# Kernel optimization log

Measured on AMD Instinct MI355X. Metric: run time of the kernel, lower is better.

## Reference

```python
import jax, jax.numpy as jnp
import numpy as np

B, N, K, ACT = 8192, 784, 16, 4  # batch, qubits/pixels, Kraus rank, d^2
L = N - 1


def setup_inputs() -> dict:
    key = jax.random.key(0)
    kx, kr, ki = jax.random.split(key, 3)
    X = jax.random.normal(kx, (B, N, 2), dtype=jnp.float32)
    # Random TPCP maps per layer via QR of a (K*4, 4) complex Gaussian (isometry method)
    M = (jax.random.normal(kr, (L, K * ACT, ACT), dtype=jnp.float32)
         + 1j * jax.random.normal(ki, (L, K * ACT, ACT), dtype=jnp.float32))
    Q, _ = jnp.linalg.qr(M)  # (L, K*4, 4), Q^dag Q = I per layer
    Kops = Q.reshape(L, K, ACT, ACT)
    return {
        "X": X,
        "kraus_real": jnp.real(Kops).astype(jnp.float32),
        "kraus_imag": jnp.imag(Kops).astype(jnp.float32),
    }


def _get_rho(x):
    # x: (B, 2) real -> pure-state density matrix (B, 2, 2)
    return jnp.einsum('bi,bj->bij', x, x)


def _tensor_product(r1, r2):
    # (B,2,2) x (B,2,2) -> (B,4,4)
    b = r1.shape[0]
    return jnp.einsum('bij,bkl->bikjl', r1, r2).reshape(b, ACT, ACT)


def _forward_layer(rho, Kl):
    # sum_k K_k rho K_k^dag ; Kl: (K,4,4), rho: (B,4,4)
    return jnp.einsum('kab,nbc,kdc->nad', Kl, rho, jnp.conj(Kl))


def _partial0(rho):
    # trace out qubit 0: (B,4,4) -> (B,2,2)
    b = rho.shape[0]
    return jnp.einsum('nacad->ncd', rho.reshape(b, 2, 2, 2, 2))


def reference(X, kraus_real, kraus_imag):
    kraus = kraus_real + 1j * kraus_imag          # (L, K, 4, 4) complex64
    X = X / jnp.linalg.norm(X, axis=-1, keepdims=True)
    Xc = X.astype(kraus.dtype)
    rho = _tensor_product(_get_rho(Xc[:, 0]), _get_rho(Xc[:, 1]))  # (B,4,4)

    def step(rho, xs):
        Kl, x = xs                                # (K,4,4), (B,2)
        rho = _forward_layer(rho, Kl)
        rho = _tensor_product(_partial0(rho), _get_rho(x))
        return rho, None

    xs = (kraus[:-1], jnp.swapaxes(Xc[:, 2:], 0, 1))  # (L-1,K,4,4), (L-1,B,2)
    rho, _ = jax.lax.scan(step, rho, xs)
    rho = _forward_layer(rho, kraus[-1])
    res = _partial0(rho)[:, 0, 0]                 # (B,) diagonal element, real-valued
    return jnp.real(res)
```

## Files before the change

kernel.cpp:

```cpp
#include <hip/hip_runtime.h>

#define L_LAYERS 783
#define L_PAD    784
#define B_BATCH  8192
#define N_SITES  784
#define K_KRAUS  16

#define SEGF     14
#define GF       56
#define TCW      36
#define PW       12

__global__ void __launch_bounds__(256)
build_T(const float* __restrict__ kr, const float* __restrict__ ki,
        float* __restrict__ Tc) {
    __shared__ float lr[K_KRAUS * 16];
    __shared__ float li[K_KRAUS * 16];
    __shared__ float gr[32], gi[32];
    int l = blockIdx.x;
    int t = threadIdx.x;
    float* o = Tc + (size_t)l * TCW;

    if (l >= L_LAYERS) {
        if (t < 12) {
            int r3 = t >> 2, col = t & 3;
            int row = (r3 == 0) ? 0 : r3 + 1;
            o[t]      = (col == row) ? 1.f : 0.f;
            o[12 + t] = 0.f;
            o[24 + t] = 0.f;
        }
        return;
    }

    lr[t] = kr[(size_t)l * 256 + t];
    li[t] = ki[(size_t)l * 256 + t];
    __syncthreads();

    if (t < 128) {
        int e = t >> 2, chunk = t & 3;
        int ci = e >> 4;
        int c = 0, d = ci;
        int m = (e >> 2) & 3, q = e & 3;
        int i1 = m >> 1, j1 = m & 1, i2 = q >> 1, j2 = q & 1;
        int off1 = c * 4 + 2 * i1 + i2;
        int off2 = d * 4 + 2 * j1 + j2;
        float ar = 0.f, ai = 0.f;
        #pragma unroll
        for (int kk = 0; kk < 4; ++kk) {
            int kbase = (chunk * 4 + kk) * 16;
            #pragma unroll
            for (int a = 0; a < 2; ++a) {
                int x1 = kbase + a * 8 + off1;
                int x2 = kbase + a * 8 + off2;
                float k1r = lr[x1], k1i = li[x1];
                float k2r = lr[x2], k2i = li[x2];
                ar += k1r * k2r + k1i * k2i;
                ai += k1i * k2r - k1r * k2i;
            }
        }
        ar += __shfl_xor(ar, 1); ar += __shfl_xor(ar, 2);
        ai += __shfl_xor(ai, 1); ai += __shfl_xor(ai, 2);
        if (chunk == 0) { gr[e] = ar; gi[e] = ai; }
    }
    __syncthreads();

    if (t < 12) {
        int r3 = t >> 2, col = t & 3;
        int row = (r3 == 0) ? 0 : r3 + 1;
        int ci = (row == 0) ? 0 : 1;
        int base = ci * 16;
        float Ur[4], Ui[4];
        #pragma unroll
        for (int q = 0; q < 4; ++q) {
            if (col == 0)      { Ur[q] = gr[base + q];      Ui[q] = gi[base + q]; }
            else if (col == 1) { Ur[q] = gr[base + 12 + q]; Ui[q] = gi[base + 12 + q]; }
            else {
                float t1r = gr[base + 4 + q], t1i = gi[base + 4 + q];
                float t2r = gr[base + 8 + q], t2i = gi[base + 8 + q];
                if (col == 2) { Ur[q] = t1r + t2r;    Ui[q] = t1i + t2i; }
                else          { Ur[q] = -(t1i - t2i); Ui[q] = t1r - t2r; }
            }
        }
        float A, Bc, Cc;
        if (row == 3) { A = Ui[0]; Bc = Ui[1] + Ui[2]; Cc = Ui[3]; }
        else          { A = Ur[0]; Bc = Ur[1] + Ur[2]; Cc = Ur[3]; }
        o[t]      = Cc;
        o[12 + t] = A - Cc;
        o[24 + t] = Bc;
    }
}

__global__ void __launch_bounds__(256, 4)
seg_fused(const float* __restrict__ X, const float* __restrict__ Tc,
          float* __restrict__ P) {
    __shared__ float2 xxs[256 * SEGF];
    int t  = threadIdx.x;
    int s  = blockIdx.y;
    int ls = s * SEGF;
    int b0 = blockIdx.x * 256;
    const float* tl0 = Tc + (size_t)ls * TCW;
    const float2* Xp = (const float2*)X;

    #pragma unroll
    for (int e = 0; e < SEGF; ++e) {
        int idx  = t + e * 256;
        int row  = idx / SEGF;
        int col  = idx - row * SEGF;
        int site = ls + 1 + col;
        site = site < (N_SITES - 1) ? site : (N_SITES - 1);
        float2 xv = Xp[(size_t)(b0 + row) * N_SITES + site];
        float inv = __builtin_amdgcn_rcpf(fmaf(xv.x, xv.x, xv.y * xv.y));
        xxs[row * SEGF + col] = make_float2(xv.x * xv.x * inv, xv.x * xv.y * inv);
    }
    __syncthreads();

    float pA[12], pB[12];
    #pragma unroll
    for (int i = 0; i < 12; ++i) pA[i] = 0.f;
    pA[0] = 1.f; pA[6] = 1.f; pA[11] = 1.f;

#define STEP(SRC, DST, I)                                                       \
    {                                                                           \
        const float* tl = tl0 + (I) * TCW;               \
        float2 xx = xxs[t * SEGF + (I)];                                        \
        float R[12];                                                            \
        _Pragma("unroll")                                                       \
        for (int e = 0; e < 12; ++e)                                            \
            R[e] = fmaf(tl[24 + e], xx.y, fmaf(tl[12 + e], xx.x, tl[e]));       \
        _Pragma("unroll")                                                       \
        for (int r = 0; r < 3; ++r) {                                           \
            float Rd = R[r * 4 + 0] - R[r * 4 + 1];                             \
            float R1 = R[r * 4 + 1];                                            \
            _Pragma("unroll")                                                   \
            for (int cc = 0; cc < 4; ++cc) {                                    \
                float base = (cc < 2) ? R1 : 0.f;                               \
                DST[r * 4 + cc] =                                               \
                    fmaf(Rd, SRC[cc],                                           \
                    fmaf(R[r * 4 + 2], SRC[4 + cc],                             \
                    fmaf(R[r * 4 + 3], SRC[8 + cc], base)));                    \
            }                                                                   \
        }                                                                       \
    }

    #pragma unroll
    for (int i = 0; i < SEGF; i += 2) {
        STEP(pA, pB, i);
        STEP(pB, pA, i + 1);
    }
#undef STEP

    int b = b0 + t;
    #pragma unroll
    for (int i = 0; i < 12; ++i)
        P[((size_t)(s * PW + i)) * B_BATCH + b] = pA[i];
}

__global__ void __launch_bounds__(256)
combine56(const float* __restrict__ X, const float* __restrict__ P,
          float* __restrict__ out) {
    __shared__ float q[256][13];
    int t = threadIdx.x;
    int j = t >> 5, bl = t & 31;
    int b = blockIdx.x * 32 + bl;

    float qa[12], qb[12];
    #pragma unroll
    for (int i = 0; i < 12; ++i) qa[i] = 0.f;
    qa[0] = 1.f; qa[6] = 1.f; qa[11] = 1.f;

#define CSTEP(SRC, DST, K)                                                      \
    {                                                                           \
        float m[12];                                                            \
        _Pragma("unroll")                                                       \
        for (int i = 0; i < 12; ++i)                                            \
            m[i] = P[((size_t)((j * 7 + (K)) * PW + i)) * B_BATCH + b];         \
        _Pragma("unroll")                                                       \
        for (int r = 0; r < 3; ++r) {                                           \
            float Rd = m[r * 4 + 0] - m[r * 4 + 1];                             \
            float R1 = m[r * 4 + 1];                                            \
            _Pragma("unroll")                                                   \
            for (int cc = 0; cc < 4; ++cc) {                                    \
                float base = (cc < 2) ? R1 : 0.f;                               \
                DST[r * 4 + cc] =                                               \
                    fmaf(Rd, SRC[cc],                                           \
                    fmaf(m[r * 4 + 2], SRC[4 + cc],                             \
                    fmaf(m[r * 4 + 3], SRC[8 + cc], base)));                    \
            }                                                                   \
        }                                                                       \
    }
    CSTEP(qa, qb, 0); CSTEP(qb, qa, 1);
    CSTEP(qa, qb, 2); CSTEP(qb, qa, 3);
    CSTEP(qa, qb, 4); CSTEP(qb, qa, 5);
    CSTEP(qa, qb, 6);
#undef CSTEP

    #pragma unroll
    for (int i = 0; i < 12; ++i) q[t][i] = qb[i];
    __syncthreads();

    if (t < 32) {
        int b2 = blockIdx.x * 32 + t;
        const float2* Xp = (const float2*)X;
        float2 xv = Xp[(size_t)b2 * N_SITES];
        float inv = __builtin_amdgcn_rcpf(fmaf(xv.x, xv.x, xv.y * xv.y));
        float v0 = xv.x * xv.x * inv;
        float v1 = xv.y * xv.y * inv;
        float v2 = xv.x * xv.y * inv;
        float v3 = 0.f;
        #pragma unroll
        for (int jj = 0; jj < 8; ++jj) {
            const float* qq = q[jj * 32 + t];
            float n0 = fmaf(qq[0], v0, fmaf(qq[1], v1, fmaf(qq[2],  v2, qq[3]  * v3)));
            float n2 = fmaf(qq[4], v0, fmaf(qq[5], v1, fmaf(qq[6],  v2, qq[7]  * v3)));
            float n3 = fmaf(qq[8], v0, fmaf(qq[9], v1, fmaf(qq[10], v2, qq[11] * v3)));
            float n1 = (v0 + v1) - n0;
            v0 = n0; v1 = n1; v2 = n2; v3 = n3;
        }
        out[b2] = v0;
    }
}

extern "C" void kernel_launch(void* const* d_in, const int* in_sizes, int n_in,
                              void* d_out, int out_size, void* d_ws, size_t ws_size,
                              hipStream_t stream) {
    const float* X  = (const float*)d_in[0];
    const float* kr = (const float*)d_in[1];
    const float* ki = (const float*)d_in[2];
    float* out = (float*)d_out;

    float* Tc = (float*)d_ws;
    const size_t Tb = ((size_t)L_PAD * TCW * sizeof(float) + 255) & ~(size_t)255;
    float* P = (float*)((char*)d_ws + Tb);

    build_T<<<L_PAD, 256, 0, stream>>>(kr, ki, Tc);

    dim3 gs(B_BATCH / 256, GF);
    seg_fused<<<gs, 256, 0, stream>>>(X, Tc, P);

    combine56<<<B_BATCH / 32, 256, 0, stream>>>(X, P, out);
}
```

Before: 37.93 us.

## Split each segment across two half-blocks and store partial products as float4

Each block now handles 128 batch rows. The two halves of the block each chain 7 layers of the 14-layer segment, so the serial dependency per thread is halved. The second half's partial product goes through shared memory and is multiplied in by the first half. P is stored and read as float4 rows in both seg_fused and combine56, and launch bounds are raised to 7 blocks per SM for occupancy. This adds a second barrier and leaves half the threads idle during the final merge.

```diff
diff --git a/kernel.cpp b/kernel.cpp
--- a/kernel.cpp
+++ b/kernel.cpp
@@ -7,9 +7,10 @@
 #define K_KRAUS  16
 
 #define SEGF     14
+#define HSEG     7
 #define GF       56
 #define TCW      36
-#define PW       12
+#define BPB      128
 
 __global__ void __launch_bounds__(256)
 build_T(const float* __restrict__ kr, const float* __restrict__ ki,
@@ -90,29 +91,33 @@
     }
 }
 
-__global__ void __launch_bounds__(256, 4)
+__global__ void __launch_bounds__(256, 7)
 seg_fused(const float* __restrict__ X, const float* __restrict__ Tc,
           float* __restrict__ P) {
-    __shared__ float2 xxs[256 * SEGF];
+    __shared__ float2 xxs[BPB * 15];
+    __shared__ float  qx[BPB][13];
     int t  = threadIdx.x;
     int s  = blockIdx.y;
     int ls = s * SEGF;
-    int b0 = blockIdx.x * 256;
-    const float* tl0 = Tc + (size_t)ls * TCW;
+    int b0 = blockIdx.x * BPB;
     const float2* Xp = (const float2*)X;
 
     #pragma unroll
-    for (int e = 0; e < SEGF; ++e) {
+    for (int e = 0; e < 7; ++e) {
         int idx  = t + e * 256;
-        int row  = idx / SEGF;
-        int col  = idx - row * SEGF;
+        int row  = idx / 14;
+        int col  = idx - row * 14;
         int site = ls + 1 + col;
         site = site < (N_SITES - 1) ? site : (N_SITES - 1);
         float2 xv = Xp[(size_t)(b0 + row) * N_SITES + site];
         float inv = __builtin_amdgcn_rcpf(fmaf(xv.x, xv.x, xv.y * xv.y));
-        xxs[row * SEGF + col] = make_float2(xv.x * xv.x * inv, xv.x * xv.y * inv);
-    }
-    __syncthreads();
+        xxs[row * 15 + col] = make_float2(xv.x * xv.x * inv, xv.x * xv.y * inv);
+    }
+    __syncthreads();
+
+    int half = t >> 7;
+    int bt   = t & (BPB - 1);
+    const float* tlh = Tc + (size_t)(ls + half * HSEG) * TCW;
 
     float pA[12], pB[12];
     #pragma unroll
@@ -121,8 +126,8 @@
 
 #define STEP(SRC, DST, I)                                                       \
     {                                                                           \
-        const float* tl = tl0 + (I) * TCW;               \
-        float2 xx = xxs[t * SEGF + (I)];                                        \
+        const float* tl = tlh + (I) * TCW;               \
+        float2 xx = xxs[bt * 15 + half * HSEG + (I)];                           \
         float R[12];                                                            \
         _Pragma("unroll")                                                       \
         for (int e = 0; e < 12; ++e)                                            \
@@ -142,17 +147,43 @@
         }                                                                       \
     }
 
-    #pragma unroll
-    for (int i = 0; i < SEGF; i += 2) {
-        STEP(pA, pB, i);
-        STEP(pB, pA, i + 1);
-    }
+    STEP(pA, pB, 0); STEP(pB, pA, 1);
+    STEP(pA, pB, 2); STEP(pB, pA, 3);
+    STEP(pA, pB, 4); STEP(pB, pA, 5);
+    STEP(pA, pB, 6);
 #undef STEP
 
-    int b = b0 + t;
-    #pragma unroll
-    for (int i = 0; i < 12; ++i)
-        P[((size_t)(s * PW + i)) * B_BATCH + b] = pA[i];
+    if (half == 1) {
+        #pragma unroll
+        for (int i = 0; i < 12; ++i) qx[bt][i] = pB[i];
+    }
+    __syncthreads();
+
+    if (half == 0) {
+        float m[12];
+        #pragma unroll
+        for (int i = 0; i < 12; ++i) m[i] = qx[bt][i];
+        float q[12];
+        #pragma unroll
+        for (int r = 0; r < 3; ++r) {
+            float Rd = m[r * 4 + 0] - m[r * 4 + 1];
+            float R1 = m[r * 4 + 1];
+            #pragma unroll
+            for (int cc = 0; cc < 4; ++cc) {
+                float base = (cc < 2) ? R1 : 0.f;
+                q[r * 4 + cc] =
+                    fmaf(Rd, pB[cc],
+                    fmaf(m[r * 4 + 2], pB[4 + cc],
+                    fmaf(m[r * 4 + 3], pB[8 + cc], base)));
+            }
+        }
+        int b = b0 + bt;
+        float4* P4 = (float4*)P;
+        #pragma unroll
+        for (int k = 0; k < 3; ++k)
+            P4[((size_t)(s * 3 + k)) * B_BATCH + b] =
+                make_float4(q[4 * k], q[4 * k + 1], q[4 * k + 2], q[4 * k + 3]);
+    }
 }
 
 __global__ void __launch_bounds__(256)
@@ -162,6 +193,7 @@
     int t = threadIdx.x;
     int j = t >> 5, bl = t & 31;
     int b = blockIdx.x * 32 + bl;
+    const float4* P4 = (const float4*)P;
 
     float qa[12], qb[12];
     #pragma unroll
@@ -172,8 +204,11 @@
     {                                                                           \
         float m[12];                                                            \
         _Pragma("unroll")                                                       \
-        for (int i = 0; i < 12; ++i)                                            \
-            m[i] = P[((size_t)((j * 7 + (K)) * PW + i)) * B_BATCH + b];         \
+        for (int k = 0; k < 3; ++k) {                                           \
+            float4 mv = P4[((size_t)((j * 7 + (K)) * 3 + k)) * B_BATCH + b];    \
+            m[4 * k + 0] = mv.x; m[4 * k + 1] = mv.y;                           \
+            m[4 * k + 2] = mv.z; m[4 * k + 3] = mv.w;                           \
+        }                                                                       \
         _Pragma("unroll")                                                       \
         for (int r = 0; r < 3; ++r) {                                           \
             float Rd = m[r * 4 + 0] - m[r * 4 + 1];                             \
@@ -234,7 +269,7 @@
 
     build_T<<<L_PAD, 256, 0, stream>>>(kr, ki, Tc);
 
-    dim3 gs(B_BATCH / 256, GF);
+    dim3 gs(B_BATCH / BPB, GF);
     seg_fused<<<gs, 256, 0, stream>>>(X, Tc, P);
 
     combine56<<<B_BATCH / 32, 256, 0, stream>>>(X, P, out);
```

Measured after the change: 114.3 us. 201% more time.
